# Kernel optimization log

Hardware: AMD Instinct MI355X
Metric: run time of the kernel (lower is better)

Reference implementation:

```python
import jax, jax.numpy as jnp
import numpy as np

RADIUS = 0.2
K_SAMPLES = 32
SPATIAL_STRIDE = 2
TEMPORAL_K = 3
BN_EPS = 1e-5


def setup_inputs() -> dict:
    key = jax.random.key(0)
    ks = jax.random.split(key, 5)
    B, L, N, C = 4, 8, 2048, 32
    mid, out = 64, 128
    xyzs = jax.random.uniform(ks[0], (B, L, N, 3), dtype=jnp.float32)
    features = jax.random.normal(ks[1], (B, L, C, N), dtype=jnp.float32)
    conv_d_w = jax.random.normal(ks[2], (mid, 3), dtype=jnp.float32) * 0.3
    conv_f_w = jax.random.normal(ks[3], (mid, C), dtype=jnp.float32) * 0.1
    bn_gamma = jnp.ones((TEMPORAL_K * mid,), jnp.float32)
    bn_beta = jnp.zeros((TEMPORAL_K * mid,), jnp.float32)
    temporal_w = jax.random.normal(ks[4], (out, TEMPORAL_K * mid), dtype=jnp.float32) * 0.05
    return {"xyzs": xyzs, "features": features, "conv_d_w": conv_d_w,
            "conv_f_w": conv_f_w, "bn_gamma": bn_gamma, "bn_beta": bn_beta,
            "temporal_w": temporal_w}


def _fps(xyz, m):
    # furthest point sampling: xyz (N,3) -> (m,) int32 indices, first index is 0
    n = xyz.shape[0]
    def body(carry, _):
        dists, last = carry
        d = jnp.sum((xyz - xyz[last]) ** 2, axis=-1)
        dists = jnp.minimum(dists, d)
        nxt = jnp.argmax(dists).astype(jnp.int32)
        return (dists, nxt), last
    init = (jnp.full((n,), jnp.finfo(xyz.dtype).max, xyz.dtype), jnp.array(0, jnp.int32))
    _, idx = jax.lax.scan(body, init, None, length=m)
    return idx


def _ball_query(anchor, neighbor):
    # anchor (M,3), neighbor (N,3) -> (M,K) int32; first K points within RADIUS,
    # missing slots filled with first valid index (0 if none), matching pointnet2.
    n = neighbor.shape[0]
    d2 = jnp.sum((anchor[:, None, :] - neighbor[None, :, :]) ** 2, axis=-1)  # (M,N)
    cand = jnp.where(d2 < RADIUS * RADIUS, jnp.arange(n, dtype=jnp.int32)[None, :], n)
    cand = jnp.sort(cand, axis=1)[:, :K_SAMPLES]  # first K in index order
    first = cand[:, 0]
    safe_first = jnp.where(first == n, 0, first)
    return jnp.where(cand == n, safe_first[:, None], cand)


def _group(pts, idx):
    # pts (BL, N, D), idx (BL, M, K) -> (BL, M, K, D)
    return jnp.take_along_axis(pts[:, None, :, :], idx[..., None], axis=2)


def _forward(xyzs, features, conv_d_w, conv_f_w, bn_gamma, bn_beta, temporal_w):
    B, L, N, _ = xyzs.shape
    C = features.shape[2]
    M = N // SPATIAL_STRIDE
    KM = bn_gamma.shape[0]  # TEMPORAL_K * mid

    # temporal zero padding [1,1]
    xp = jnp.concatenate([jnp.zeros((B, 1, N, 3), xyzs.dtype), xyzs,
                          jnp.zeros((B, 1, N, 3), xyzs.dtype)], axis=1)  # (B,L+2,N,3)
    fp = jnp.concatenate([jnp.zeros((B, 1, C, N), features.dtype), features,
                          jnp.zeros((B, 1, C, N), features.dtype)], axis=1)

    # anchors from each center frame t=1..L
    center = xp[:, 1:L + 1].reshape(B * L, N, 3)
    anchor_idx = jax.vmap(lambda x: _fps(x, M))(center)            # (BL, M)
    anchor = jnp.take_along_axis(center, anchor_idx[..., None], axis=1)  # (BL, M, 3)

    offset_feats = []
    for o in range(TEMPORAL_K):  # neighbor frames t-1, t, t+1
        nb = xp[:, o:o + L].reshape(B * L, N, 3)
        nf = jnp.swapaxes(fp[:, o:o + L].reshape(B * L, C, N), 1, 2)  # (BL,N,C)
        idx = jax.vmap(_ball_query)(anchor, nb)                      # (BL,M,K)
        g_xyz = _group(nb, idx)                                      # (BL,M,K,3)
        g_f = _group(nf, idx)                                        # (BL,M,K,C)
        disp = g_xyz - anchor[:, :, None, :]
        d_out = jnp.einsum('oc,bmkc->bmko', conv_d_w, disp)          # (BL,M,K,mid)
        f_out = jnp.einsum('oc,bmkc->bmko', conv_f_w, g_f)
        # multiplication aggregation + sum pooling over neighbors
        offset_feats.append(jnp.sum(f_out * d_out, axis=2))          # (BL,M,mid)

    x = jnp.concatenate(offset_feats, axis=-1)                       # (BL,M,KM)
    x = jnp.transpose(x.reshape(B, L, M, KM), (0, 1, 3, 2))          # (B,L,KM,M)

    # BatchNorm1d applied per frame (torch loop calls BN once per t): stats over (B, M)
    mean = jnp.mean(x, axis=(0, 3), keepdims=True)
    var = jnp.var(x, axis=(0, 3), keepdims=True)
    x = (x - mean) * jax.lax.rsqrt(var + BN_EPS)
    x = x * bn_gamma[None, None, :, None] + bn_beta[None, None, :, None]
    x = jax.nn.relu(x)

    new_features = jnp.einsum('ok,blkm->blom', temporal_w, x)        # (B,L,out,M)
    new_xyzs = anchor.reshape(B, L, M, 3)
    return new_xyzs, new_features


def reference(xyzs, features, conv_d_w, conv_f_w, bn_gamma, bn_beta, temporal_w):
    return _forward(xyzs, features, conv_d_w, conv_f_w, bn_gamma, bn_beta, temporal_w)
```

## Files before the change

### kernel.cpp

```cpp
#include <hip/hip_runtime.h>

#define NB_B 4
#define NB_L 8
#define NB_N 2048
#define NB_C 32
#define NB_M 1024

#define ANCH_OFF  0
#define FT_OFF    98304
#define XRAW_OFF  2195456
#define STATS_OFF 8486912

__global__ __launch_bounds__(256) void transpose_kernel(const float* __restrict__ f,
                                                        float* __restrict__ ft) {
  __shared__ float tile[NB_C][65];
  int frame = blockIdx.x >> 5;
  int n0 = (blockIdx.x & 31) * 64;
  int t = threadIdx.x;
  const float* src = f + (size_t)frame * NB_C * NB_N;
#pragma unroll
  for (int i = 0; i < 8; ++i) {
    int q = t + i * 256;
    int c = q >> 6, n = q & 63;
    tile[c][n] = src[c * NB_N + n0 + n];
  }
  __syncthreads();
  float* dst = ft + ((size_t)frame * NB_N + n0) * NB_C;
  int n = t >> 2, c0 = (t & 3) * 8;
  float v[8];
#pragma unroll
  for (int i = 0; i < 8; ++i) v[i] = tile[c0 + i][n];
  float4 w0 = {v[0], v[1], v[2], v[3]};
  float4 w1 = {v[4], v[5], v[6], v[7]};
  *(float4*)(dst + n * NB_C + c0) = w0;
  *(float4*)(dst + n * NB_C + c0 + 4) = w1;
}

__device__ __forceinline__ unsigned long long umax64(unsigned long long a,
                                                     unsigned long long b) {
  return a > b ? a : b;
}

template <int CTRL>
__device__ __forceinline__ unsigned long long dpp_xch64(unsigned long long v) {
  int lo = (int)(unsigned)v;
  int hi = (int)(unsigned)(v >> 32);
  int plo = __builtin_amdgcn_update_dpp(0, lo, CTRL, 0xF, 0xF, false);
  int phi = __builtin_amdgcn_update_dpp(0, hi, CTRL, 0xF, 0xF, false);
  return ((unsigned long long)(unsigned)phi << 32) | (unsigned)plo;
}

#define DPP_XOR1 0xB1
#define DPP_XOR2 0x4E
#define DPP_HMIR 0x141
#define DPP_MIR  0x140

#define FPS_T 512

__global__ __launch_bounds__(FPS_T) void fps_kernel(const float* __restrict__ xyzs,
                                                    float* __restrict__ anchors,
                                                    float* __restrict__ d_out) {
  int cloud = blockIdx.x;
  int t = threadIdx.x;
  int w = t >> 6;
  int lane = t & 63;
  const float* xyz = xyzs + (size_t)cloud * NB_N * 3;
  __shared__ float4 pos4[NB_N];
  __shared__ __align__(16) unsigned long long slots32[2][32];
  __shared__ int hist[NB_M];
  for (int i = t; i < NB_N; i += FPS_T) {
    float x = xyz[i * 3 + 0];
    float y = xyz[i * 3 + 1];
    float z = xyz[i * 3 + 2];
    pos4[i] = make_float4(x, y, z, 0.f);
  }
  __syncthreads();
  float px[4], py[4], pz[4], dist[4];
  unsigned inv[4];
#pragma unroll
  for (int j = 0; j < 4; ++j) {
    int n = j * FPS_T + t;
    float4 p = pos4[n];
    px[j] = p.x; py[j] = p.y; pz[j] = p.z;
    dist[j] = 3.402823466e38f;
    inv[j] = 0x7FFFFFFFu - (unsigned)n;
  }
  int last = 0;
  float4 sp = pos4[0];
  float lx = sp.x, ly = sp.y, lz = sp.z;
  int sidx = w * 4 + (lane >> 4);
  bool swrite = (lane & 15) == 0;
  for (int m = 0; m < NB_M; ++m) {
    if (t == 0) hist[m] = last;
    int par = m & 1;
    unsigned long long best = 0;
#pragma unroll
    for (int j = 0; j < 4; ++j) {
      float dx = __fsub_rn(px[j], lx);
      float dy = __fsub_rn(py[j], ly);
      float dz = __fsub_rn(pz[j], lz);
      float d = __fadd_rn(__fadd_rn(__fmul_rn(dx, dx), __fmul_rn(dy, dy)),
                          __fmul_rn(dz, dz));
      float dj = fminf(dist[j], d);
      dist[j] = dj;
      unsigned long long pk =
          ((unsigned long long)__float_as_uint(dj) << 32) | inv[j];
      best = umax64(best, pk);
    }
    best = umax64(best, dpp_xch64<DPP_XOR1>(best));
    best = umax64(best, dpp_xch64<DPP_XOR2>(best));
    best = umax64(best, dpp_xch64<DPP_HMIR>(best));
    best = umax64(best, dpp_xch64<DPP_MIR>(best));
    if (swrite) slots32[par][sidx] = best;
    __syncthreads();
    ulonglong2 pr2 = *(const ulonglong2*)&slots32[par][(lane & 15) * 2];
    unsigned long long g = umax64(pr2.x, pr2.y);
    g = umax64(g, dpp_xch64<DPP_XOR1>(g));
    g = umax64(g, dpp_xch64<DPP_XOR2>(g));
    g = umax64(g, dpp_xch64<DPP_HMIR>(g));
    g = umax64(g, dpp_xch64<DPP_MIR>(g));
    last = 0x7FFFFFFF - (int)(unsigned)g;
    float4 p = pos4[last];
    lx = p.x; ly = p.y; lz = p.z;
  }
  __syncthreads();
  for (int mm = t; mm < NB_M; mm += FPS_T) {
    int idx = hist[mm];
    float4 p = pos4[idx];
    size_t o = ((size_t)cloud * NB_M + mm) * 3;
    anchors[o + 0] = p.x; anchors[o + 1] = p.y; anchors[o + 2] = p.z;
    d_out[o + 0] = p.x;   d_out[o + 1] = p.y;   d_out[o + 2] = p.z;
  }
}

__device__ __forceinline__ float rdlane(float v, int l) {
  return __int_as_float(__builtin_amdgcn_readlane(__float_as_int(v), l));
}

#define BQ_WAVES 4
#define BQ_TPW 4

__global__ __launch_bounds__(256) void bq_conv_kernel(
    const float* __restrict__ xyzs, const float* __restrict__ ft,
    const float* __restrict__ anchors, const float* __restrict__ conv_d_w,
    const float* __restrict__ conv_f_w, float* __restrict__ x_raw) {
  int w = threadIdx.x >> 6, lane = threadIdx.x & 63;
  int gw = blockIdx.x * BQ_WAVES + w;
  int task0 = gw * BQ_TPW;
  int cloud = task0 / 3072;
  int rem = task0 - cloud * 3072;
  int o = rem >> 10, m0 = rem & 1023;
  int b = cloud >> 3, l = cloud & 7;
  int nl = l + o - 1;
  __shared__ int list_s[BQ_WAVES][32];
  float* xbase = x_raw + ((size_t)(l * NB_B + b) * NB_M + m0) * 192 + o * 64;
  if (nl < 0 || nl >= NB_L) {
#pragma unroll
    for (int t4 = 0; t4 < BQ_TPW; ++t4) xbase[(size_t)t4 * 192 + lane] = 0.0f;
    return;
  }
  const float4* wf4 = (const float4*)(conv_f_w + lane * 32);
  float wf[32];
#pragma unroll
  for (int i = 0; i < 8; ++i) {
    float4 v = wf4[i];
    wf[i * 4 + 0] = v.x; wf[i * 4 + 1] = v.y;
    wf[i * 4 + 2] = v.z; wf[i * 4 + 3] = v.w;
  }
  float wd0 = conv_d_w[lane * 3 + 0];
  float wd1 = conv_d_w[lane * 3 + 1];
  float wd2 = conv_d_w[lane * 3 + 2];

  const float* nb = xyzs + (size_t)(b * NB_L + nl) * NB_N * 3;
  const float* ftf = ft + (size_t)(b * NB_L + nl) * NB_N * NB_C + (lane & 31);
  unsigned long long lmlt = (1ull << lane) - 1ull;
  int kbase = (lane >> 5) << 4;

  for (int t4 = 0; t4 < BQ_TPW; ++t4) {
    int m = m0 + t4;
    const float* ap = anchors + ((size_t)cloud * NB_M + m) * 3;
    float ax = ap[0], ay = ap[1], az = ap[2];

    int count = 0;
    for (int batch = 0; batch < 4; ++batch) {
      unsigned long long bm[8];
#pragma unroll
      for (int c2 = 0; c2 < 8; ++c2) {
        int n = batch * 512 + c2 * 64 + lane;
        float x = nb[n * 3 + 0], y = nb[n * 3 + 1], z = nb[n * 3 + 2];
        float dx = __fsub_rn(ax, x);
        float dy = __fsub_rn(ay, y);
        float dz = __fsub_rn(az, z);
        float d2 = __fadd_rn(__fadd_rn(__fmul_rn(dx, dx), __fmul_rn(dy, dy)),
                             __fmul_rn(dz, dz));
        bm[c2] = __ballot(d2 < 0.04f);
      }
#pragma unroll
      for (int c2 = 0; c2 < 8; ++c2) {
        bool hit = (bm[c2] >> lane) & 1;
        int pos = count + __popcll(bm[c2] & lmlt);
        if (hit && pos < 32) list_s[w][pos] = batch * 512 + c2 * 64 + lane;
        count += __popcll(bm[c2]);
      }
      if (count >= 32) break;
    }
    asm volatile("s_waitcnt lgkmcnt(0)" ::: "memory");
    int cnt = count < 32 ? count : 32;
    int first = (cnt > 0) ? list_s[w][0] : 0;

    int k = lane & 31;
    int idxk = (k < cnt) ? list_s[w][k] : first;
    float bx = nb[idxk * 3 + 0], by = nb[idxk * 3 + 1], bz = nb[idxk * 3 + 2];
    float d0 = __fsub_rn(bx, ax);
    float d1 = __fsub_rn(by, ay);
    float d2v = __fsub_rn(bz, az);

    float G0 = 0.f, G1 = 0.f, G2 = 0.f;
#pragma unroll 8
    for (int i = 0; i < 16; ++i) {
      int kk = kbase + i;
      int ik = (kk < cnt) ? list_s[w][kk] : first;
      float fv = ftf[(size_t)ik * NB_C];
      float e0 = __shfl(d0, kk);
      float e1 = __shfl(d1, kk);
      float e2 = __shfl(d2v, kk);
      G0 = fmaf(fv, e0, G0);
      G1 = fmaf(fv, e1, G1);
      G2 = fmaf(fv, e2, G2);
    }
    G0 += __shfl_xor(G0, 32);
    G1 += __shfl_xor(G1, 32);
    G2 += __shfl_xor(G2, 32);

    float acc = 0.f;
#pragma unroll
    for (int cc = 0; cc < 32; ++cc) {
      float g0 = rdlane(G0, cc);
      float g1 = rdlane(G1, cc);
      float g2 = rdlane(G2, cc);
      float tt = fmaf(g2, wd2, fmaf(g1, wd1, g0 * wd0));
      acc = fmaf(wf[cc], tt, acc);
    }
    xbase[(size_t)t4 * 192 + lane] = acc;
  }
}

__global__ __launch_bounds__(192) void bn_stats_kernel(const float* __restrict__ x_raw,
                                                       float* __restrict__ stats) {
  int bid = blockIdx.x;
  int mt = bid & 3, bb = (bid >> 2) & 3, l = bid >> 4;
  int c = threadIdx.x;
  const float* p = x_raw + ((size_t)(l * NB_B + bb) * NB_M + mt * 256) * 192 + c;
  float s = 0.f, s2 = 0.f;
  for (int i = 0; i < 256; ++i) {
    float v = p[(size_t)i * 192];
    s += v;
    s2 = fmaf(v, v, s2);
  }
  atomicAdd(&stats[l * 192 + c], s);
  atomicAdd(&stats[1536 + l * 192 + c], s2);
}

__global__ __launch_bounds__(256) void final_kernel(
    const float* __restrict__ x_raw, const float* __restrict__ stats,
    const float* __restrict__ gamma, const float* __restrict__ beta,
    const float* __restrict__ tw, float* __restrict__ out) {
  __shared__ __align__(16) float xn[32 * 192];
  __shared__ __align__(16) float wt[64 * 132];
  __shared__ float sc[192], sh[192];
  int cloud = blockIdx.x >> 5;
  int mt = blockIdx.x & 31;
  int b = cloud >> 3, l = cloud & 7;
  int m0 = mt * 32;
  int t = threadIdx.x;
  if (t < 192) {
    float mean = stats[l * 192 + t] * (1.0f / 4096.0f);
    float ex2 = stats[1536 + l * 192 + t] * (1.0f / 4096.0f);
    float var = fmaxf(ex2 - mean * mean, 0.0f);
    float g = gamma[t] / sqrtf(var + 1e-5f);
    sc[t] = g;
    sh[t] = fmaf(-mean, g, beta[t]);
  }
  __syncthreads();
  const float* xp = x_raw + ((size_t)(l * NB_B + b) * NB_M + m0) * 192;
#pragma unroll
  for (int i = 0; i < 24; ++i) {
    int q = t + i * 256;
    int cc = q % 192;
    float v = xp[q];
    xn[q] = fmaxf(fmaf(v, sc[cc], sh[cc]), 0.0f);
  }
  float acc[4][4];
#pragma unroll
  for (int i = 0; i < 4; ++i)
#pragma unroll
    for (int j = 0; j < 4; ++j) acc[i][j] = 0.f;
  int o0 = (t & 31) * 4;
  int mg = (t >> 5) * 4;
  for (int kt = 0; kt < 3; ++kt) {
    __syncthreads();
#pragma unroll
    for (int i = 0; i < 32; ++i) {
      int q = t + i * 256;
      int oo = q >> 6, kk = q & 63;
      wt[kk * 132 + oo] = tw[oo * 192 + kt * 64 + kk];
    }
    __syncthreads();
#pragma unroll
    for (int kk = 0; kk < 64; kk += 4) {
      float a[4][4], bb2[4][4];
#pragma unroll
      for (int mi = 0; mi < 4; ++mi) {
        float4 v = *(const float4*)&xn[(mg + mi) * 192 + kt * 64 + kk];
        a[mi][0] = v.x; a[mi][1] = v.y; a[mi][2] = v.z; a[mi][3] = v.w;
      }
#pragma unroll
      for (int j = 0; j < 4; ++j) {
        float4 v = *(const float4*)&wt[(kk + j) * 132 + o0];
        bb2[j][0] = v.x; bb2[j][1] = v.y; bb2[j][2] = v.z; bb2[j][3] = v.w;
      }
#pragma unroll
      for (int mi = 0; mi < 4; ++mi)
#pragma unroll
        for (int j = 0; j < 4; ++j)
#pragma unroll
          for (int oi = 0; oi < 4; ++oi)
            acc[mi][oi] = fmaf(a[mi][j], bb2[j][oi], acc[mi][oi]);
    }
  }
  float* op = out + 98304 + ((size_t)cloud * 128 + o0) * NB_M + m0 + mg;
#pragma unroll
  for (int oi = 0; oi < 4; ++oi) {
    float4 v = {acc[0][oi], acc[1][oi], acc[2][oi], acc[3][oi]};
    *(float4*)(op + (size_t)oi * NB_M) = v;
  }
}

extern "C" void kernel_launch(void* const* d_in, const int* in_sizes, int n_in,
                              void* d_out, int out_size, void* d_ws, size_t ws_size,
                              hipStream_t stream) {
  const float* xyzs = (const float*)d_in[0];
  const float* features = (const float*)d_in[1];
  const float* conv_d_w = (const float*)d_in[2];
  const float* conv_f_w = (const float*)d_in[3];
  const float* bn_gamma = (const float*)d_in[4];
  const float* bn_beta = (const float*)d_in[5];
  const float* temporal_w = (const float*)d_in[6];
  float* ws = (float*)d_ws;
  float* anchors = ws + ANCH_OFF;
  float* ft = ws + FT_OFF;
  float* xraw = ws + XRAW_OFF;
  float* stats = ws + STATS_OFF;
  float* out = (float*)d_out;

  hipMemsetAsync(stats, 0, 3072 * sizeof(float), stream);
  transpose_kernel<<<1024, 256, 0, stream>>>(features, ft);
  fps_kernel<<<32, FPS_T, 0, stream>>>(xyzs, anchors, out);
  bq_conv_kernel<<<6144, 256, 0, stream>>>(xyzs, ft, anchors, conv_d_w,
                                           conv_f_w, xraw);
  bn_stats_kernel<<<128, 192, 0, stream>>>(xraw, stats);
  final_kernel<<<1024, 256, 0, stream>>>(xraw, stats, bn_gamma, bn_beta,
                                         temporal_w, out);
}
```

Before: 770.9 us.

## Fuse transpose into FPS kernel, use f64 min/max for packed argmax

Merges the feature transpose into the FPS launch as extra blocks so it can run alongside the 32 long-running FPS blocks, removing one launch and the serialization between them. FPS now keeps the packed (distance, inverse index) key as a double and uses hardware f64 fmin/fmax in place of 64-bit integer compares, and it records the sampled-index history in registers instead of shared memory. The ball-query kernel stages displacements in shared memory and reads them as float4 instead of using three shuffles per neighbor. The f64 ordering trick relies on nonnegative distances packed into the high bits, and the transpose blocks now launch 512 threads with half of them idle.

```diff
diff --git a/kernel.cpp b/kernel.cpp
--- a/kernel.cpp
+++ b/kernel.cpp
@@ -11,43 +11,14 @@
 #define XRAW_OFF  2195456
 #define STATS_OFF 8486912
 
-__global__ __launch_bounds__(256) void transpose_kernel(const float* __restrict__ f,
-                                                        float* __restrict__ ft) {
-  __shared__ float tile[NB_C][65];
-  int frame = blockIdx.x >> 5;
-  int n0 = (blockIdx.x & 31) * 64;
-  int t = threadIdx.x;
-  const float* src = f + (size_t)frame * NB_C * NB_N;
-#pragma unroll
-  for (int i = 0; i < 8; ++i) {
-    int q = t + i * 256;
-    int c = q >> 6, n = q & 63;
-    tile[c][n] = src[c * NB_N + n0 + n];
-  }
-  __syncthreads();
-  float* dst = ft + ((size_t)frame * NB_N + n0) * NB_C;
-  int n = t >> 2, c0 = (t & 3) * 8;
-  float v[8];
-#pragma unroll
-  for (int i = 0; i < 8; ++i) v[i] = tile[c0 + i][n];
-  float4 w0 = {v[0], v[1], v[2], v[3]};
-  float4 w1 = {v[4], v[5], v[6], v[7]};
-  *(float4*)(dst + n * NB_C + c0) = w0;
-  *(float4*)(dst + n * NB_C + c0 + 4) = w1;
-}
-
-__device__ __forceinline__ unsigned long long umax64(unsigned long long a,
-                                                     unsigned long long b) {
-  return a > b ? a : b;
-}
-
-template <int CTRL>
-__device__ __forceinline__ unsigned long long dpp_xch64(unsigned long long v) {
-  int lo = (int)(unsigned)v;
-  int hi = (int)(unsigned)(v >> 32);
-  int plo = __builtin_amdgcn_update_dpp(0, lo, CTRL, 0xF, 0xF, false);
-  int phi = __builtin_amdgcn_update_dpp(0, hi, CTRL, 0xF, 0xF, false);
-  return ((unsigned long long)(unsigned)phi << 32) | (unsigned)plo;
+__device__ __forceinline__ double u2d(unsigned long long u) {
+  return __longlong_as_double((long long)u);
+}
+__device__ __forceinline__ unsigned long long d2u(double d) {
+  return (unsigned long long)__double_as_longlong(d);
+}
+__device__ __forceinline__ double pack_dk(float d, unsigned inv) {
+  return u2d(((unsigned long long)__float_as_uint(d) << 32) | inv);
 }
 
 #define DPP_XOR1 0xB1
@@ -55,19 +26,56 @@
 #define DPP_HMIR 0x141
 #define DPP_MIR  0x140
 
+template <int CTRL>
+__device__ __forceinline__ double dpp_max_f64(double v) {
+  int lo = __double2loint(v), hi = __double2hiint(v);
+  int plo = __builtin_amdgcn_update_dpp(0, lo, CTRL, 0xF, 0xF, false);
+  int phi = __builtin_amdgcn_update_dpp(0, hi, CTRL, 0xF, 0xF, false);
+  return fmax(v, __hiloint2double(phi, plo));
+}
+
 #define FPS_T 512
 
-__global__ __launch_bounds__(FPS_T) void fps_kernel(const float* __restrict__ xyzs,
-                                                    float* __restrict__ anchors,
-                                                    float* __restrict__ d_out) {
+__global__ __launch_bounds__(FPS_T) void fps_transpose_kernel(
+    const float* __restrict__ xyzs, const float* __restrict__ features,
+    float* __restrict__ ft, float* __restrict__ anchors,
+    float* __restrict__ d_out) {
+  __shared__ __align__(16) unsigned char smem[32 * 1024 + 512];
+  int t = threadIdx.x;
+  if (blockIdx.x >= 32) {
+    float(*tile)[65] = (float(*)[65])smem;
+    int tb = blockIdx.x - 32;
+    int frame = tb >> 5;
+    int n0 = (tb & 31) * 64;
+    const float* src = features + (size_t)frame * NB_C * NB_N;
+    if (t < 256) {
+#pragma unroll
+      for (int i = 0; i < 8; ++i) {
+        int q = t + i * 256;
+        int c = q >> 6, n = q & 63;
+        tile[c][n] = src[c * NB_N + n0 + n];
+      }
+    }
+    __syncthreads();
+    if (t < 256) {
+      float* dst = ft + ((size_t)frame * NB_N + n0) * NB_C;
+      int n = t >> 2, c0 = (t & 3) * 8;
+      float v[8];
+#pragma unroll
+      for (int i = 0; i < 8; ++i) v[i] = tile[c0 + i][n];
+      float4 w0 = {v[0], v[1], v[2], v[3]};
+      float4 w1 = {v[4], v[5], v[6], v[7]};
+      *(float4*)(dst + n * NB_C + c0) = w0;
+      *(float4*)(dst + n * NB_C + c0 + 4) = w1;
+    }
+    return;
+  }
+  float4* pos4 = (float4*)smem;
+  unsigned long long* slots = (unsigned long long*)(smem + 32768);
   int cloud = blockIdx.x;
-  int t = threadIdx.x;
   int w = t >> 6;
   int lane = t & 63;
   const float* xyz = xyzs + (size_t)cloud * NB_N * 3;
-  __shared__ float4 pos4[NB_N];
-  __shared__ __align__(16) unsigned long long slots32[2][32];
-  __shared__ int hist[NB_M];
   for (int i = t; i < NB_N; i += FPS_T) {
     float x = xyz[i * 3 + 0];
     float y = xyz[i * 3 + 1];
@@ -75,25 +83,29 @@
     pos4[i] = make_float4(x, y, z, 0.f);
   }
   __syncthreads();
-  float px[4], py[4], pz[4], dist[4];
+  float px[4], py[4], pz[4];
+  double Kd[4];
   unsigned inv[4];
 #pragma unroll
   for (int j = 0; j < 4; ++j) {
     int n = j * FPS_T + t;
     float4 p = pos4[n];
     px[j] = p.x; py[j] = p.y; pz[j] = p.z;
-    dist[j] = 3.402823466e38f;
     inv[j] = 0x7FFFFFFFu - (unsigned)n;
+    Kd[j] = pack_dk(3.402823466e38f, inv[j]);
   }
   int last = 0;
+  int h0 = 0, h1 = 0;
   float4 sp = pos4[0];
   float lx = sp.x, ly = sp.y, lz = sp.z;
   int sidx = w * 4 + (lane >> 4);
   bool swrite = (lane & 15) == 0;
+  int t512 = t + 512;
   for (int m = 0; m < NB_M; ++m) {
-    if (t == 0) hist[m] = last;
+    h0 = (m == t) ? last : h0;
+    h1 = (m == t512) ? last : h1;
     int par = m & 1;
-    unsigned long long best = 0;
+    double best = u2d(0ull);
 #pragma unroll
     for (int j = 0; j < 4; ++j) {
       float dx = __fsub_rn(px[j], lx);
@@ -101,35 +113,34 @@
       float dz = __fsub_rn(pz[j], lz);
       float d = __fadd_rn(__fadd_rn(__fmul_rn(dx, dx), __fmul_rn(dy, dy)),
                           __fmul_rn(dz, dz));
-      float dj = fminf(dist[j], d);
-      dist[j] = dj;
-      unsigned long long pk =
-          ((unsigned long long)__float_as_uint(dj) << 32) | inv[j];
-      best = umax64(best, pk);
-    }
-    best = umax64(best, dpp_xch64<DPP_XOR1>(best));
-    best = umax64(best, dpp_xch64<DPP_XOR2>(best));
-    best = umax64(best, dpp_xch64<DPP_HMIR>(best));
-    best = umax64(best, dpp_xch64<DPP_MIR>(best));
-    if (swrite) slots32[par][sidx] = best;
+      Kd[j] = fmin(Kd[j], pack_dk(d, inv[j]));
+      best = fmax(best, Kd[j]);
+    }
+    best = dpp_max_f64<DPP_XOR1>(best);
+    best = dpp_max_f64<DPP_XOR2>(best);
+    best = dpp_max_f64<DPP_HMIR>(best);
+    best = dpp_max_f64<DPP_MIR>(best);
+    if (swrite) slots[par * 32 + sidx] = d2u(best);
     __syncthreads();
-    ulonglong2 pr2 = *(const ulonglong2*)&slots32[par][(lane & 15) * 2];
-    unsigned long long g = umax64(pr2.x, pr2.y);
-    g = umax64(g, dpp_xch64<DPP_XOR1>(g));
-    g = umax64(g, dpp_xch64<DPP_XOR2>(g));
-    g = umax64(g, dpp_xch64<DPP_HMIR>(g));
-    g = umax64(g, dpp_xch64<DPP_MIR>(g));
-    last = 0x7FFFFFFF - (int)(unsigned)g;
+    ulonglong2 pr2 = *(const ulonglong2*)&slots[par * 32 + (lane & 15) * 2];
+    double g = fmax(u2d(pr2.x), u2d(pr2.y));
+    g = dpp_max_f64<DPP_XOR1>(g);
+    g = dpp_max_f64<DPP_XOR2>(g);
+    g = dpp_max_f64<DPP_HMIR>(g);
+    g = dpp_max_f64<DPP_MIR>(g);
+    last = 0x7FFFFFFF - __double2loint(g);
     float4 p = pos4[last];
     lx = p.x; ly = p.y; lz = p.z;
   }
-  __syncthreads();
-  for (int mm = t; mm < NB_M; mm += FPS_T) {
-    int idx = hist[mm];
-    float4 p = pos4[idx];
-    size_t o = ((size_t)cloud * NB_M + mm) * 3;
+  {
+    float4 p = pos4[h0];
+    size_t o = ((size_t)cloud * NB_M + t) * 3;
     anchors[o + 0] = p.x; anchors[o + 1] = p.y; anchors[o + 2] = p.z;
     d_out[o + 0] = p.x;   d_out[o + 1] = p.y;   d_out[o + 2] = p.z;
+    float4 q = pos4[h1];
+    size_t o2 = ((size_t)cloud * NB_M + t512) * 3;
+    anchors[o2 + 0] = q.x; anchors[o2 + 1] = q.y; anchors[o2 + 2] = q.z;
+    d_out[o2 + 0] = q.x;   d_out[o2 + 1] = q.y;   d_out[o2 + 2] = q.z;
   }
 }
 
@@ -153,6 +164,7 @@
   int b = cloud >> 3, l = cloud & 7;
   int nl = l + o - 1;
   __shared__ int list_s[BQ_WAVES][32];
+  __shared__ __align__(16) float disp_s[BQ_WAVES][32][4];
   float* xbase = x_raw + ((size_t)(l * NB_B + b) * NB_M + m0) * 192 + o * 64;
   if (nl < 0 || nl >= NB_L) {
 #pragma unroll
@@ -214,6 +226,8 @@
     float d0 = __fsub_rn(bx, ax);
     float d1 = __fsub_rn(by, ay);
     float d2v = __fsub_rn(bz, az);
+    if (lane < 32) *(float4*)&disp_s[w][lane][0] = make_float4(d0, d1, d2v, 0.f);
+    asm volatile("s_waitcnt lgkmcnt(0)" ::: "memory");
 
     float G0 = 0.f, G1 = 0.f, G2 = 0.f;
 #pragma unroll 8
@@ -221,12 +235,10 @@
       int kk = kbase + i;
       int ik = (kk < cnt) ? list_s[w][kk] : first;
       float fv = ftf[(size_t)ik * NB_C];
-      float e0 = __shfl(d0, kk);
-      float e1 = __shfl(d1, kk);
-      float e2 = __shfl(d2v, kk);
-      G0 = fmaf(fv, e0, G0);
-      G1 = fmaf(fv, e1, G1);
-      G2 = fmaf(fv, e2, G2);
+      float4 dd = *(const float4*)&disp_s[w][kk][0];
+      G0 = fmaf(fv, dd.x, G0);
+      G1 = fmaf(fv, dd.y, G1);
+      G2 = fmaf(fv, dd.z, G2);
     }
     G0 += __shfl_xor(G0, 32);
     G1 += __shfl_xor(G1, 32);
@@ -354,8 +366,8 @@
   float* out = (float*)d_out;
 
   hipMemsetAsync(stats, 0, 3072 * sizeof(float), stream);
-  transpose_kernel<<<1024, 256, 0, stream>>>(features, ft);
-  fps_kernel<<<32, FPS_T, 0, stream>>>(xyzs, anchors, out);
+  fps_transpose_kernel<<<1056, FPS_T, 0, stream>>>(xyzs, features, ft,
+                                                   anchors, out);
   bq_conv_kernel<<<6144, 256, 0, stream>>>(xyzs, ft, anchors, conv_d_w,
                                            conv_f_w, xraw);
   bn_stats_kernel<<<128, 192, 0, stream>>>(xraw, stats);
```

After: 744.3 us. 1.04x faster.
